# Performance work log

Hardware: AMD Instinct MI355X
Metric: run time of the kernel (lower is better)

Reference implementation:

```python
import jax, jax.numpy as jnp
import numpy as np

L, D, H, DH, W, G, FF = 2, 768, 12, 64, 256, 64, 3072  # W = one-sided window (attention_window=512)
B, S = 2, 4096
NEG = -1e9


def setup_inputs() -> dict:
    key = jax.random.key(0)
    ks = jax.random.split(key, 16)
    inp = {}
    inp['hidden_states'] = jax.random.normal(ks[0], (B, S, D), jnp.float32)
    # HF Longformer convention: <0 masked, >0 global, 0 local. First G tokens are global.
    inp['attention_mask'] = jnp.zeros((B, S), jnp.float32).at[:, :G].set(1.0)
    inp['padding_len'] = 0
    inp['level_hierarchy'] = 0
    def w(k, shape):
        return (jax.random.normal(k, shape, jnp.float32) * 0.02)
    for i, n in enumerate(['Wq', 'Wk', 'Wv', 'Wqg', 'Wkg', 'Wvg', 'Wo']):
        inp[n] = w(ks[1 + i], (L, D, D))
        inp['b' + n[1:].lower()] = jnp.zeros((L, D), jnp.float32)
    inp['Wi'] = w(ks[8], (L, D, FF)); inp['bi'] = jnp.zeros((L, FF), jnp.float32)
    inp['Wo2'] = w(ks[9], (L, FF, D)); inp['bo2'] = jnp.zeros((L, D), jnp.float32)
    for n in ['ln1', 'ln2']:
        inp[n + '_g'] = jnp.ones((L, D), jnp.float32)
        inp[n + '_b'] = jnp.zeros((L, D), jnp.float32)
    return inp


def _ln(x, g, b):
    mu = jnp.mean(x, -1, keepdims=True)
    var = jnp.mean(jnp.square(x - mu), -1, keepdims=True)
    return (x - mu) * jax.lax.rsqrt(var + 1e-5) * g + b


def _chunk3(x, nc, w):
    # x: [..., S, d] -> [..., nc, 3w, d]: keys of chunks (c-1, c, c+1), zero-padded at the ends
    shp = x.shape
    xr = x.reshape(shp[:-2] + (nc, w, shp[-1]))
    pad = [(0, 0)] * xr.ndim
    pad[-3] = (1, 1)
    xp = jnp.pad(xr, pad)
    return jnp.concatenate([xp[..., :-2, :, :], xp[..., 1:-1, :, :], xp[..., 2:, :, :]], axis=-2)


def _layer(h, mask, Wq, bq, Wk, bk, Wv, bv, Wqg, bqg, Wkg, bkg, Wvg, bvg,
           Wo, bo, ln1_g, ln1_b, Wi, bi, Wo2, bo2, ln2_g, ln2_b):
    Bb, Ss, Dd = h.shape
    nc = Ss // W
    scale = 1.0 / np.sqrt(DH)
    def heads(x):
        return x.reshape(Bb, Ss, H, DH).transpose(0, 2, 1, 3)  # [B,H,S,dh]
    q = heads(h @ Wq + bq) * scale
    k = heads(h @ Wk + bk)
    v = heads(h @ Wv + bv)
    # --- sliding-window (banded) attention, chunked ---
    qc = q.reshape(Bb, H, nc, W, DH)
    k3 = _chunk3(k, nc, W)  # [B,H,nc,3W,dh]
    v3 = _chunk3(v, nc, W)
    local = jnp.einsum('bhcid,bhcjd->bhcij', qc, k3)  # [B,H,nc,W,3W]
    i = jnp.arange(W)[:, None]
    j = jnp.arange(3 * W)[None, :]
    band_ok = jnp.abs(j - W - i) <= W                              # [W,3W]
    keypos = jnp.arange(nc)[:, None, None] * W + (j - W)[None]     # [nc,1,3W]
    in_range = (keypos >= 0) & (keypos < Ss)
    # masked and global keys are removed from the windowed attention (handled via global cols)
    key_local = _chunk3((mask == 0).astype(h.dtype)[..., None], nc, W)[..., 0] > 0.5  # [B,nc,3W]
    valid = band_ok[None, None] & in_range[None] & key_local[:, :, None, :]  # [B,nc,W,3W]
    local = jnp.where(valid[:, None], local, NEG)
    # --- global key columns (every token attends to the G global tokens) ---
    kg, vg = k[:, :, :G], v[:, :, :G]
    sg = jnp.einsum('bhsd,bhgd->bhsg', q, kg).reshape(Bb, H, nc, W, G)
    probs = jax.nn.softmax(jnp.concatenate([sg, local], axis=-1), axis=-1)
    pg, pl = probs[..., :G], probs[..., G:]
    out = (jnp.einsum('bhcig,bhgd->bhcid', pg, vg)
           + jnp.einsum('bhcij,bhcjd->bhcid', pl, v3)).reshape(Bb, H, Ss, DH)
    # --- global token rows: full attention with dedicated global projections ---
    qg = heads(h @ Wqg + bqg)[:, :, :G] * scale
    kgf = heads(h @ Wkg + bkg)
    vgf = heads(h @ Wvg + bvg)
    add = jnp.where(mask < 0, NEG, 0.0)[:, None, None, :]
    pgl = jax.nn.softmax(jnp.einsum('bhgd,bhsd->bhgs', qg, kgf) + add, axis=-1)
    out = out.at[:, :, :G].set(jnp.einsum('bhgs,bhsd->bhgd', pgl, vgf))
    out = jnp.where((mask < 0)[:, None, :, None], 0.0, out)
    attn = out.transpose(0, 2, 1, 3).reshape(Bb, Ss, Dd) @ Wo + bo
    h = _ln(attn + h, ln1_g, ln1_b)
    ff = jax.nn.gelu(h @ Wi + bi, approximate=False) @ Wo2 + bo2
    return _ln(ff + h, ln2_g, ln2_b)


def reference(hidden_states, attention_mask, padding_len, level_hierarchy,
              Wq, bq, Wk, bk, Wv, bv, Wqg, bqg, Wkg, bkg, Wvg, bvg,
              Wo, bo, ln1_g, ln1_b, Wi, bi, Wo2, bo2, ln2_g, ln2_b):
    h = hidden_states
    for l in range(L):
        h = _layer(h, attention_mask,
                   Wq[l], bq[l], Wk[l], bk[l], Wv[l], bv[l],
                   Wqg[l], bqg[l], Wkg[l], bkg[l], Wvg[l], bvg[l],
                   Wo[l], bo[l], ln1_g[l], ln1_b[l],
                   Wi[l], bi[l], Wo2[l], bo2[l], ln2_g[l], ln2_b[l])
    if padding_len > 0:
        h = h[:, :-padding_len]
    return h
```

## Files before the change

### kernel.cpp

```cpp
#include <hip/hip_runtime.h>

#define B_ 2
#define S_ 4096
#define D_ 768
#define H_ 12
#define DH_ 64
#define W_ 256
#define G_ 64
#define FF_ 3072
#define L_ 2
#define M_ (B_*S_)
#define NEGV -1e9f
#define NSPLIT 16

typedef short bf16x8 __attribute__((ext_vector_type(8)));
typedef float f32x4 __attribute__((ext_vector_type(4)));
typedef unsigned short u16;
typedef unsigned short u16x4 __attribute__((ext_vector_type(4)));

__device__ __forceinline__ u16 f2bf(float f) {
  union { float f; unsigned u; } a; a.f = f;
  unsigned r = a.u + 0x7FFFu + ((a.u >> 16) & 1u);
  return (u16)(r >> 16);
}

__device__ __forceinline__ f32x4 mfma16(bf16x8 a, bf16x8 b, f32x4 c) {
  return __builtin_amdgcn_mfma_f32_16x16x32_bf16(a, b, c, 0, 0, 0);
}

__device__ __forceinline__ void gload16(const u16* g, u16* l) {
  __builtin_amdgcn_global_load_lds((const __attribute__((address_space(1))) void*)g,
                                   (__attribute__((address_space(3))) void*)l, 16, 0, 0);
}

__device__ __forceinline__ int xcd_swz(int bid, int nwg) {
  if ((nwg & 7) == 0) {
    int cpx = nwg >> 3;
    bid = (bid & 7) * cpx + (bid >> 3);
  }
  return bid;
}

struct Ptr7 { const float* p[7]; };
__global__ __launch_bounds__(256) void wtrans7(Ptr7 in, u16* __restrict__ out) {
  __shared__ float tile[32][33];
  int z = blockIdx.z;
  int slab = z >> 1, l = z & 1;
  const float* src = in.p[slab] + (size_t)l * D_ * D_;
  u16* dst = out + (size_t)z * D_ * D_;
  int k0 = blockIdx.y * 32, n0 = blockIdx.x * 32;
  int tx = threadIdx.x, ty = threadIdx.y;
#pragma unroll
  for (int i = 0; i < 4; i++)
    tile[ty + i*8][tx] = src[(size_t)(k0 + ty + i*8) * D_ + n0 + tx];
  __syncthreads();
#pragma unroll
  for (int i = 0; i < 4; i++)
    dst[(size_t)(n0 + ty + i*8) * D_ + k0 + tx] = f2bf(tile[tx][ty + i*8]);
}

__global__ __launch_bounds__(256) void wtrans(const float* __restrict__ in,
                                              u16* __restrict__ out, int K, int N) {
  __shared__ float tile[32][33];
  size_t base = (size_t)blockIdx.z * K * N;
  int k0 = blockIdx.y * 32, n0 = blockIdx.x * 32;
  int tx = threadIdx.x, ty = threadIdx.y;
#pragma unroll
  for (int i = 0; i < 4; i++)
    tile[ty + i*8][tx] = in[base + (size_t)(k0 + ty + i*8) * N + n0 + tx];
  __syncthreads();
#pragma unroll
  for (int i = 0; i < 4; i++)
    out[base + (size_t)(n0 + ty + i*8) * K + k0 + tx] = f2bf(tile[tx][ty + i*8]);
}

__global__ __launch_bounds__(256) void copyconv(const float* __restrict__ in,
                                                float* __restrict__ outf,
                                                u16* __restrict__ outb, int n4) {
  int i = blockIdx.x * 256 + threadIdx.x;
  if (i >= n4) return;
  float4 v = ((const float4*)in)[i];
  ((float4*)outf)[i] = v;
  u16x4 o;
  o[0] = f2bf(v.x); o[1] = f2bf(v.y); o[2] = f2bf(v.z); o[3] = f2bf(v.w);
  ((u16x4*)outb)[i] = o;
}

template <int MODE>
__global__ __launch_bounds__(256) void gemm_lds(const u16* __restrict__ A,
                                                const u16* __restrict__ Bt,
                                                const float* __restrict__ bias,
                                                float* __restrict__ Cf,
                                                u16* __restrict__ Cb,
                                                int Ndim, int Kdim, int rowTileStride) {
  __shared__ u16 lA[128 * 64];
  __shared__ u16 lB[128 * 64];
  int gx = gridDim.x;
  int bid = blockIdx.x + blockIdx.y * gx;
  bid = xcd_swz(bid, gx * gridDim.y);
  int bm = (bid / gx) * rowTileStride * 128;
  int bn = (bid % gx) * 128;
  int tid = threadIdx.x;
  int lane = tid & 63, w = tid >> 6;
  int r0w = (w >> 1) * 64, c0w = (w & 1) * 64;
  int lr = lane & 15, lg = lane >> 4;
  int srow = tid >> 3;
  int scol = ((tid & 7) ^ (srow & 7)) * 8;
  u16* ldst = (u16*)0;

  f32x4 acc[4][4] = {};
  for (int k0 = 0; k0 < Kdim; k0 += 64) {
#pragma unroll
    for (int p = 0; p < 4; p++) {
      gload16(A + (size_t)(bm + p * 32 + srow) * Kdim + k0 + scol, lA + p * 2048 + tid * 8);
      gload16(Bt + (size_t)(bn + p * 32 + srow) * Kdim + k0 + scol, lB + p * 2048 + tid * 8);
    }
    __syncthreads();
    bf16x8 a[2][4], b[2][4];
#pragma unroll
    for (int ks = 0; ks < 2; ks++)
#pragma unroll
      for (int i = 0; i < 4; i++) {
        int row = r0w + i * 16 + lr;
        int c8 = ks * 4 + lg;
        a[ks][i] = *(const bf16x8*)&lA[row * 64 + ((c8 ^ (row & 7)) * 8)];
        int rowb = c0w + i * 16 + lr;
        b[ks][i] = *(const bf16x8*)&lB[rowb * 64 + ((c8 ^ (rowb & 7)) * 8)];
      }
#pragma unroll
    for (int ks = 0; ks < 2; ks++)
#pragma unroll
      for (int i = 0; i < 4; i++)
#pragma unroll
        for (int j = 0; j < 4; j++)
          acc[i][j] = mfma16(a[ks][i], b[ks][j], acc[i][j]);
    __syncthreads();
  }
  (void)ldst;

  int r0 = bm + r0w, c0 = bn + c0w;
  int cr = (lane >> 4) * 4, cc = lane & 15;
#pragma unroll
  for (int j = 0; j < 4; j++) {
    int col = c0 + j * 16 + cc;
    float bv = bias[col];
#pragma unroll
    for (int i = 0; i < 4; i++) {
#pragma unroll
      for (int r = 0; r < 4; r++) {
        size_t off = (size_t)(r0 + i * 16 + cr + r) * Ndim + col;
        float v = acc[i][j][r] + bv;
        if (MODE == 0) Cf[off] = v;
        else if (MODE == 1) Cb[off] = f2bf(v);
        else if (MODE == 2) Cb[off] = f2bf(v * 0.125f);
        else Cb[off] = f2bf(0.5f * v * (1.0f + erff(v * 0.70710678118f)));
      }
    }
  }
}

struct Bias5 { const float* p[5]; };
__global__ __launch_bounds__(256) void gemm_qkv(const u16* __restrict__ A,
                                                const u16* __restrict__ Wt,
                                                Bias5 bp,
                                                u16* __restrict__ OutBase,
                                                int l) {
  __shared__ u16 lA[128 * 64];
  __shared__ u16 lB[128 * 64];
  int bid = blockIdx.x + blockIdx.y * 30;
  bid = xcd_swz(bid, 1920);
  int bx = bid % 30, by = bid / 30;
  int widx = bx / 6;
  int bn = (bx % 6) * 128;
  int bm = by * 128;
  int slab = widx + (widx >= 3 ? 1 : 0);
  const size_t DD = (size_t)D_ * D_;
  const u16* Bt = Wt + ((size_t)slab * L_ + l) * DD;
  u16* Cb = OutBase + (size_t)slab * M_ * D_;
  const float* bias = bp.p[widx];
  int tid = threadIdx.x;
  int lane = tid & 63, w = tid >> 6;
  int r0w = (w >> 1) * 64, c0w = (w & 1) * 64;
  int lr = lane & 15, lg = lane >> 4;
  int srow = tid >> 3;
  int scol = ((tid & 7) ^ (srow & 7)) * 8;

  f32x4 acc[4][4] = {};
  for (int k0 = 0; k0 < D_; k0 += 64) {
#pragma unroll
    for (int p = 0; p < 4; p++) {
      gload16(A + (size_t)(bm + p * 32 + srow) * D_ + k0 + scol, lA + p * 2048 + tid * 8);
      gload16(Bt + (size_t)(bn + p * 32 + srow) * D_ + k0 + scol, lB + p * 2048 + tid * 8);
    }
    __syncthreads();
    bf16x8 a[2][4], b[2][4];
#pragma unroll
    for (int ks = 0; ks < 2; ks++)
#pragma unroll
      for (int i = 0; i < 4; i++) {
        int row = r0w + i * 16 + lr;
        int c8 = ks * 4 + lg;
        a[ks][i] = *(const bf16x8*)&lA[row * 64 + ((c8 ^ (row & 7)) * 8)];
        int rowb = c0w + i * 16 + lr;
        b[ks][i] = *(const bf16x8*)&lB[rowb * 64 + ((c8 ^ (rowb & 7)) * 8)];
      }
#pragma unroll
    for (int ks = 0; ks < 2; ks++)
#pragma unroll
      for (int i = 0; i < 4; i++)
#pragma unroll
        for (int j = 0; j < 4; j++)
          acc[i][j] = mfma16(a[ks][i], b[ks][j], acc[i][j]);
    __syncthreads();
  }

  int r0 = bm + r0w, c0 = bn + c0w;
  int cr = (lane >> 4) * 4, cc = lane & 15;
  float scale = (widx == 0) ? 0.125f : 1.0f;
#pragma unroll
  for (int j = 0; j < 4; j++) {
    int col = c0 + j * 16 + cc;
    float bv = bias[col];
#pragma unroll
    for (int i = 0; i < 4; i++) {
#pragma unroll
      for (int r = 0; r < 4; r++) {
        size_t off = (size_t)(r0 + i * 16 + cr + r) * D_ + col;
        Cb[off] = f2bf((acc[i][j][r] + bv) * scale);
      }
    }
  }
}

__global__ __launch_bounds__(128) void attn_local(const u16* __restrict__ qb,
                                                  const u16* __restrict__ kb_,
                                                  const u16* __restrict__ vb,
                                                  const float* __restrict__ mask,
                                                  u16* __restrict__ ao) {
  int bid = blockIdx.x + blockIdx.y * gridDim.x;
  bid = xcd_swz(bid, 1536);
  int cx = bid & 63, bh = bid >> 6;
  int c = cx >> 2, sub = cx & 3;
  int b = bh / H_, h = bh % H_;
  int tid = threadIdx.x;
  int w = tid >> 6, lane = tid & 63;
  int lr = lane & 15, lg = lane >> 4;

  __shared__ u16 vtT[64][72];
  __shared__ u16 plds[2][32][72];
  __shared__ unsigned char vflag[576];

  int base_off = sub * 64;
  int kwin0 = c * W_ - W_;
  for (int i = tid; i < 576; i += 128) {
    int kp = kwin0 + base_off + i;
    vflag[i] = (kp >= 0 && kp < S_ && mask[b * S_ + kp] == 0.0f) ? 1 : 0;
  }

  size_t hoff = (size_t)b * S_ * D_ + h * DH_;
  int qrow0 = c * W_ + base_off + w * 32;
  bf16x8 aq[2][2];
#pragma unroll
  for (int fi = 0; fi < 2; fi++)
#pragma unroll
    for (int ks = 0; ks < 2; ks++)
      aq[fi][ks] = *(const bf16x8*)(qb + hoff + (size_t)(qrow0 + fi * 16 + lr) * D_ + ks * 32 + lg * 8);

  float ls[2][4];
  f32x4 o[2][4] = {};
#pragma unroll
  for (int fi = 0; fi < 2; fi++)
#pragma unroll
    for (int r = 0; r < 4; r++) ls[fi][r] = 0.f;

  int stg_k4 = tid >> 3, stg_j = tid & 7;
  int stg_dh0 = stg_j * 8;

  for (int kb = 0; kb <= 9; kb++) {
    int kstart = 0;
    if (kb > 0) {
      kstart = kwin0 + base_off + (kb - 1) * 64;
      if (kstart + 64 <= 0 || kstart >= S_) continue;
    }
    __syncthreads();
    {
#pragma unroll
      for (int p = 0; p < 4; p++) {
        int key = p * 16 + stg_k4;
        int kp = (kb ? kstart : 0) + key;
        bf16x8 row = *(const bf16x8*)(vb + hoff + (size_t)kp * D_ + stg_dh0);
        u16* basep = &vtT[stg_dh0][key ^ (stg_j << 3)];
#pragma unroll
        for (int e = 0; e < 8; e++) basep[e * 72] = (u16)row[e];
      }
    }
    __syncthreads();

    bf16x8 bk0[4], bk1[4];
#pragma unroll
    for (int nj = 0; nj < 4; nj++) {
      int kp = (kb ? kstart : 0) + nj * 16 + lr;
      const u16* ks8 = kb_ + hoff + (size_t)kp * D_ + lg * 8;
      bk0[nj] = *(const bf16x8*)(ks8);
      bk1[nj] = *(const bf16x8*)(ks8 + 32);
    }
    f32x4 sc[2][4];
#pragma unroll
    for (int fi = 0; fi < 2; fi++)
#pragma unroll
      for (int nj = 0; nj < 4; nj++) {
        f32x4 t = {};
        t = mfma16(aq[fi][0], bk0[nj], t);
        t = mfma16(aq[fi][1], bk1[nj], t);
        sc[fi][nj] = t;
      }

    if (kb >= 2 && kb <= 8) {
#pragma unroll
      for (int nj = 0; nj < 4; nj++) {
        bool kv = vflag[(kb - 1) * 64 + nj * 16 + lr] != 0;
#pragma unroll
        for (int fi = 0; fi < 2; fi++)
#pragma unroll
          for (int r = 0; r < 4; r++)
            sc[fi][nj][r] = kv ? sc[fi][nj][r] : NEGV;
      }
    } else if (kb > 0) {
#pragma unroll
      for (int nj = 0; nj < 4; nj++) {
        int fidx = (kb - 1) * 64 + nj * 16 + lr;
        int koff = base_off + fidx;
        bool kv = vflag[fidx] != 0;
#pragma unroll
        for (int fi = 0; fi < 2; fi++)
#pragma unroll
          for (int r = 0; r < 4; r++) {
            int wq = base_off + w * 32 + fi * 16 + lg * 4 + r;
            if (!(kv && koff >= wq && koff <= wq + 2 * W_)) sc[fi][nj][r] = NEGV;
          }
      }
    }

#pragma unroll
    for (int fi = 0; fi < 2; fi++)
#pragma unroll
      for (int r = 0; r < 4; r++) {
        float ps = 0.f;
#pragma unroll
        for (int nj = 0; nj < 4; nj++) {
          float p = __expf(sc[fi][nj][r]);
          sc[fi][nj][r] = p;
          ps += p;
        }
#pragma unroll
        for (int d = 1; d < 16; d <<= 1) ps += __shfl_xor(ps, d);
        ls[fi][r] += ps;
      }

#pragma unroll
    for (int fi = 0; fi < 2; fi++)
#pragma unroll
      for (int nj = 0; nj < 4; nj++)
#pragma unroll
        for (int r = 0; r < 4; r++)
          plds[w][fi * 16 + lg * 4 + r][nj * 16 + lr] = f2bf(sc[fi][nj][r]);
    asm volatile("s_waitcnt lgkmcnt(0)" ::: "memory");
    __builtin_amdgcn_sched_barrier(0);

    bf16x8 ap[2][2];
#pragma unroll
    for (int fi = 0; fi < 2; fi++)
#pragma unroll
      for (int ks = 0; ks < 2; ks++)
        ap[fi][ks] = *(const bf16x8*)&plds[w][fi * 16 + lr][ks * 32 + lg * 8];
#pragma unroll
    for (int dj = 0; dj < 4; dj++) {
      int xr = ((dj * 16 + lr) >> 3) & 7;
#pragma unroll
      for (int ks = 0; ks < 2; ks++) {
        bf16x8 bv = *(const bf16x8*)&vtT[dj * 16 + lr][(ks * 32 + lg * 8) ^ (xr << 3)];
        o[0][dj] = mfma16(ap[0][ks], bv, o[0][dj]);
        o[1][dj] = mfma16(ap[1][ks], bv, o[1][dj]);
      }
    }
  }

#pragma unroll
  for (int fi = 0; fi < 2; fi++)
#pragma unroll
    for (int dj = 0; dj < 4; dj++)
#pragma unroll
      for (int r = 0; r < 4; r++) {
        int row = qrow0 + fi * 16 + lg * 4 + r;
        float v = o[fi][dj][r] / ls[fi][r];
        ao[hoff + (size_t)row * D_ + dj * 16 + lr] = f2bf(v);
      }
}

__global__ __launch_bounds__(128) void attn_gsplit(const u16* __restrict__ qg,
                                                   const u16* __restrict__ kg,
                                                   const u16* __restrict__ vg,
                                                   float* __restrict__ opart,
                                                   float* __restrict__ lpart) {
  int sp = blockIdx.x, bh = blockIdx.y;
  int b = bh / H_, h = bh % H_;
  int tid = threadIdx.x, w = tid >> 6, lane = tid & 63;
  int lr = lane & 15, lg = lane >> 4;
  __shared__ u16 vtT[64][72];
  __shared__ u16 plds[2][32][72];
  size_t hoff = (size_t)b * S_ * D_ + h * DH_;
  int qrow0 = w * 32;
  bf16x8 aq[2][2];
#pragma unroll
  for (int fi = 0; fi < 2; fi++)
#pragma unroll
    for (int ks = 0; ks < 2; ks++)
      aq[fi][ks] = *(const bf16x8*)(qg + hoff + (size_t)(qrow0 + fi * 16 + lr) * D_ + ks * 32 + lg * 8);
  float ls[2][4];
  f32x4 o[2][4] = {};
#pragma unroll
  for (int fi = 0; fi < 2; fi++)
#pragma unroll
    for (int r = 0; r < 4; r++) ls[fi][r] = 0.f;

  int stg_k4 = tid >> 3, stg_j = tid & 7;
  int stg_dh0 = stg_j * 8;

  for (int kb = 0; kb < 4; kb++) {
    int kstart = sp * 256 + kb * 64;
    __syncthreads();
#pragma unroll
    for (int p = 0; p < 4; p++) {
      int key = p * 16 + stg_k4;
      bf16x8 row = *(const bf16x8*)(vg + hoff + (size_t)(kstart + key) * D_ + stg_dh0);
      u16* basep = &vtT[stg_dh0][key ^ (stg_j << 3)];
#pragma unroll
      for (int e = 0; e < 8; e++) basep[e * 72] = (u16)row[e];
    }
    __syncthreads();

    bf16x8 bk0[4], bk1[4];
#pragma unroll
    for (int nj = 0; nj < 4; nj++) {
      const u16* ks8 = kg + hoff + (size_t)(kstart + nj * 16 + lr) * D_ + lg * 8;
      bk0[nj] = *(const bf16x8*)(ks8);
      bk1[nj] = *(const bf16x8*)(ks8 + 32);
    }
    f32x4 sc[2][4];
#pragma unroll
    for (int fi = 0; fi < 2; fi++)
#pragma unroll
      for (int nj = 0; nj < 4; nj++) {
        f32x4 t = {};
        t = mfma16(aq[fi][0], bk0[nj], t);
        t = mfma16(aq[fi][1], bk1[nj], t);
        sc[fi][nj] = t;
      }
#pragma unroll
    for (int fi = 0; fi < 2; fi++)
#pragma unroll
      for (int r = 0; r < 4; r++) {
        float ps = 0.f;
#pragma unroll
        for (int nj = 0; nj < 4; nj++) {
          float p = __expf(sc[fi][nj][r]);
          sc[fi][nj][r] = p;
          ps += p;
        }
#pragma unroll
        for (int d = 1; d < 16; d <<= 1) ps += __shfl_xor(ps, d);
        ls[fi][r] += ps;
      }
#pragma unroll
    for (int fi = 0; fi < 2; fi++)
#pragma unroll
      for (int nj = 0; nj < 4; nj++)
#pragma unroll
        for (int r = 0; r < 4; r++)
          plds[w][fi * 16 + lg * 4 + r][nj * 16 + lr] = f2bf(sc[fi][nj][r]);
    asm volatile("s_waitcnt lgkmcnt(0)" ::: "memory");
    __builtin_amdgcn_sched_barrier(0);
    bf16x8 ap[2][2];
#pragma unroll
    for (int fi = 0; fi < 2; fi++)
#pragma unroll
      for (int ks = 0; ks < 2; ks++)
        ap[fi][ks] = *(const bf16x8*)&plds[w][fi * 16 + lr][ks * 32 + lg * 8];
#pragma unroll
    for (int dj = 0; dj < 4; dj++) {
      int xr = ((dj * 16 + lr) >> 3) & 7;
#pragma unroll
      for (int ks = 0; ks < 2; ks++) {
        bf16x8 bv = *(const bf16x8*)&vtT[dj * 16 + lr][(ks * 32 + lg * 8) ^ (xr << 3)];
        o[0][dj] = mfma16(ap[0][ks], bv, o[0][dj]);
        o[1][dj] = mfma16(ap[1][ks], bv, o[1][dj]);
      }
    }
  }

  size_t pbase = (size_t)(bh * NSPLIT + sp) * 64;
#pragma unroll
  for (int fi = 0; fi < 2; fi++)
#pragma unroll
    for (int r = 0; r < 4; r++) {
      int row = qrow0 + fi * 16 + lg * 4 + r;
      if (lr == 0) lpart[pbase + row] = ls[fi][r];
#pragma unroll
      for (int dj = 0; dj < 4; dj++)
        opart[(pbase + row) * 64 + dj * 16 + lr] = o[fi][dj][r];
    }
}

__global__ __launch_bounds__(256) void attn_gcombine(const float* __restrict__ opart,
                                                     const float* __restrict__ lpart,
                                                     u16* __restrict__ ao) {
  int bh = blockIdx.x;
  int b = bh / H_, h = bh % H_;
  int t = threadIdx.x;
  __shared__ float lt[64];
  if (t < 64) {
    float lsum = 0.f;
#pragma unroll
    for (int sp = 0; sp < NSPLIT; sp++)
      lsum += lpart[(size_t)(bh * NSPLIT + sp) * 64 + t];
    lt[t] = lsum;
  }
  __syncthreads();
  int row = t >> 2, c0 = (t & 3) * 16;
  float acc[16] = {};
  for (int sp = 0; sp < NSPLIT; sp++) {
    const float* op = opart + ((size_t)(bh * NSPLIT + sp) * 64 + row) * 64 + c0;
#pragma unroll
    for (int j = 0; j < 16; j++) acc[j] += op[j];
  }
  float inv = 1.f / lt[row];
  size_t hoff = (size_t)b * S_ * D_ + h * DH_;
#pragma unroll
  for (int j = 0; j < 16; j++)
    ao[hoff + (size_t)row * D_ + c0 + j] = f2bf(acc[j] * inv);
}

__global__ __launch_bounds__(256) void ln_fused(const float* __restrict__ x,
                                                const float* __restrict__ res,
                                                const float* __restrict__ gg,
                                                const float* __restrict__ bb,
                                                float* __restrict__ outf,
                                                u16* __restrict__ outb) {
  int row = blockIdx.x, t = threadIdx.x;
  const float* xr = x + (size_t)row * D_;
  const float* rr = res + (size_t)row * D_;
  float v0 = xr[t] + rr[t];
  float v1 = xr[t + 256] + rr[t + 256];
  float v2 = xr[t + 512] + rr[t + 512];
  __shared__ float sha[4], shb[4];
  float s = v0 + v1 + v2;
#pragma unroll
  for (int d = 1; d < 64; d <<= 1) s += __shfl_xor(s, d);
  if ((t & 63) == 0) sha[t >> 6] = s;
  __syncthreads();
  float mu = (sha[0] + sha[1] + sha[2] + sha[3]) * (1.f / 768.f);
  float d0 = v0 - mu, d1 = v1 - mu, d2 = v2 - mu;
  float s2 = d0 * d0 + d1 * d1 + d2 * d2;
#pragma unroll
  for (int d = 1; d < 64; d <<= 1) s2 += __shfl_xor(s2, d);
  if ((t & 63) == 0) shb[t >> 6] = s2;
  __syncthreads();
  float var = (shb[0] + shb[1] + shb[2] + shb[3]) * (1.f / 768.f);
  float rs = rsqrtf(var + 1e-5f);
  float dd[3] = {d0, d1, d2};
#pragma unroll
  for (int i = 0; i < 3; i++) {
    int col = t + i * 256;
    float y = dd[i] * rs * gg[col] + bb[col];
    outf[(size_t)row * D_ + col] = y;
    outb[(size_t)row * D_ + col] = f2bf(y);
  }
}

extern "C" void kernel_launch(void* const* d_in, const int* in_sizes, int n_in,
                              void* d_out, int out_size, void* d_ws, size_t ws_size,
                              hipStream_t stream) {
  (void)in_sizes; (void)n_in; (void)out_size; (void)ws_size;
  const float* hidden = (const float*)d_in[0];
  const float* mask   = (const float*)d_in[1];
  const float* Wq  = (const float*)d_in[4];   const float* bq  = (const float*)d_in[5];
  const float* Wk  = (const float*)d_in[6];   const float* bk  = (const float*)d_in[7];
  const float* Wv  = (const float*)d_in[8];   const float* bv  = (const float*)d_in[9];
  const float* Wqg = (const float*)d_in[10];  const float* bqg = (const float*)d_in[11];
  const float* Wkg = (const float*)d_in[12];  const float* bkg = (const float*)d_in[13];
  const float* Wvg = (const float*)d_in[14];  const float* bvg = (const float*)d_in[15];
  const float* Wo  = (const float*)d_in[16];  const float* bo  = (const float*)d_in[17];
  const float* Wi  = (const float*)d_in[18];  const float* bi  = (const float*)d_in[19];
  const float* Wo2 = (const float*)d_in[20];  const float* bo2 = (const float*)d_in[21];
  const float* ln1g = (const float*)d_in[22]; const float* ln1b = (const float*)d_in[23];
  const float* ln2g = (const float*)d_in[24]; const float* ln2b = (const float*)d_in[25];

  char* ws = (char*)d_ws;
  size_t off = 0;
  auto alloc = [&](size_t bytes) -> void* {
    void* p = ws + off;
    off += (bytes + 255) & ~(size_t)255;
    return p;
  };
  const size_t DD = (size_t)D_ * D_;
  const size_t DF = (size_t)D_ * FF_;
  u16* Wt = (u16*)alloc((7 * L_ * DD + 2 * L_ * DF) * 2);
  u16* wqg_t = Wt + 3 * L_ * DD;
  u16* wo_t  = Wt + 6 * L_ * DD;
  u16* wi_t  = Wt + 7 * L_ * DD;
  u16* wo2_t = Wt + 7 * L_ * DD + L_ * DF;

  float* hbuf  = (float*)alloc((size_t)M_ * D_ * 4);
  float* h1buf = (float*)alloc((size_t)M_ * D_ * 4);
  float* t1    = (float*)alloc((size_t)M_ * D_ * 4);
  u16* A_bf = (u16*)alloc((size_t)M_ * D_ * 2);
  u16* B_bf = (u16*)alloc((size_t)M_ * FF_ * 2);
  u16* qbf  = (u16*)alloc((size_t)M_ * D_ * 2);
  u16* kbf  = (u16*)alloc((size_t)M_ * D_ * 2);
  u16* vbf  = (u16*)alloc((size_t)M_ * D_ * 2);
  u16* qgbf = (u16*)alloc((size_t)M_ * D_ * 2);
  u16* kgbf = (u16*)alloc((size_t)M_ * D_ * 2);
  u16* vgbf = (u16*)alloc((size_t)M_ * D_ * 2);
  u16* aobf = (u16*)alloc((size_t)M_ * D_ * 2);
  float* opart = (float*)alloc((size_t)B_ * H_ * NSPLIT * 64 * 64 * 4);
  float* lpart = (float*)alloc((size_t)B_ * H_ * NSPLIT * 64 * 4);

  dim3 tb(32, 8);
  Ptr7 wp;
  wp.p[0] = Wq; wp.p[1] = Wk; wp.p[2] = Wv; wp.p[3] = Wqg;
  wp.p[4] = Wkg; wp.p[5] = Wvg; wp.p[6] = Wo;
  wtrans7<<<dim3(24, 24, 14), tb, 0, stream>>>(wp, Wt);
  wtrans<<<dim3(96, 24, 2), tb, 0, stream>>>(Wi,  wi_t,  D_, FF_);
  wtrans<<<dim3(24, 96, 2), tb, 0, stream>>>(Wo2, wo2_t, FF_, D_);

  copyconv<<<(M_ * D_ / 4 + 255) / 256, 256, 0, stream>>>(hidden, hbuf, A_bf, M_ * D_ / 4);

  for (int l = 0; l < L_; l++) {
    size_t wdd = (size_t)l * DD;
    size_t wdf = (size_t)l * DF;
    dim3 g64(6, 64), g2(6, 2), gff(24, 64);

    Bias5 bp;
    bp.p[0] = bq  + l * D_;
    bp.p[1] = bk  + l * D_;
    bp.p[2] = bv  + l * D_;
    bp.p[3] = bkg + l * D_;
    bp.p[4] = bvg + l * D_;
    gemm_qkv<<<dim3(30, 64), 256, 0, stream>>>(A_bf, Wt, bp, qbf, l);
    gemm_lds<2><<<g2, 256, 0, stream>>>(A_bf, wqg_t + wdd, bqg + l * D_, nullptr, qgbf, D_, D_, 32);

    attn_local<<<dim3((S_ / W_) * 4, B_ * H_), 128, 0, stream>>>(qbf, kbf, vbf, mask, aobf);
    attn_gsplit<<<dim3(NSPLIT, B_ * H_), 128, 0, stream>>>(qgbf, kgbf, vgbf, opart, lpart);
    attn_gcombine<<<B_ * H_, 256, 0, stream>>>(opart, lpart, aobf);

    gemm_lds<0><<<g64, 256, 0, stream>>>(aobf, wo_t + wdd, bo + l * D_, t1, nullptr, D_, D_, 1);
    ln_fused<<<M_, 256, 0, stream>>>(t1, hbuf, ln1g + l * D_, ln1b + l * D_, h1buf, A_bf);

    gemm_lds<3><<<gff, 256, 0, stream>>>(A_bf, wi_t + wdf, bi + l * FF_, nullptr, B_bf, FF_, D_, 1);
    gemm_lds<0><<<g64, 256, 0, stream>>>(B_bf, wo2_t + wdf, bo2 + l * D_, t1, nullptr, D_, FF_, 1);

    float* outp = (l == L_ - 1) ? (float*)d_out : hbuf;
    ln_fused<<<M_, 256, 0, stream>>>(t1, h1buf, ln2g + l * D_, ln2b + l * D_, outp, A_bf);
  }
}
```

Before: 767.6 us.

## Double-buffer GEMM K loop, keep residual stream in bf16, use tanh GELU

The GEMM kernels now load the next K slice into a second LDS buffer while MFMAs run on the current one. The K step drops to 32 with a remapped swizzle, and waits use vmcnt plus raw barriers. The residual stream and GEMM outputs are stored as bf16 instead of fp32, and LayerNorm reads bf16 with vectorized loads, so far fewer bytes move between kernels. Exact erf GELU is replaced by a tanh approximation. Together these cut memory traffic and stall time, at the cost of lower precision in the residual path and in the GELU.

```diff
diff --git a/kernel.cpp b/kernel.cpp
--- a/kernel.cpp
+++ b/kernel.cpp
@@ -23,6 +23,10 @@
   unsigned r = a.u + 0x7FFFu + ((a.u >> 16) & 1u);
   return (u16)(r >> 16);
 }
+__device__ __forceinline__ float b2f(u16 u) {
+  union { unsigned u; float f; } a; a.u = ((unsigned)u) << 16;
+  return a.f;
+}
 
 __device__ __forceinline__ f32x4 mfma16(bf16x8 a, bf16x8 b, f32x4 c) {
   return __builtin_amdgcn_mfma_f32_16x16x32_bf16(a, b, c, 0, 0, 0);
@@ -74,27 +78,35 @@
     out[base + (size_t)(n0 + ty + i*8) * K + k0 + tx] = f2bf(tile[tx][ty + i*8]);
 }
 
-__global__ __launch_bounds__(256) void copyconv(const float* __restrict__ in,
-                                                float* __restrict__ outf,
-                                                u16* __restrict__ outb, int n4) {
+__global__ __launch_bounds__(256) void conv_b(const float* __restrict__ in,
+                                              u16* __restrict__ outb, int n4) {
   int i = blockIdx.x * 256 + threadIdx.x;
   if (i >= n4) return;
   float4 v = ((const float4*)in)[i];
-  ((float4*)outf)[i] = v;
   u16x4 o;
   o[0] = f2bf(v.x); o[1] = f2bf(v.y); o[2] = f2bf(v.z); o[3] = f2bf(v.w);
   ((u16x4*)outb)[i] = o;
 }
 
 template <int MODE>
-__global__ __launch_bounds__(256) void gemm_lds(const u16* __restrict__ A,
-                                                const u16* __restrict__ Bt,
-                                                const float* __restrict__ bias,
-                                                float* __restrict__ Cf,
-                                                u16* __restrict__ Cb,
-                                                int Ndim, int Kdim, int rowTileStride) {
-  __shared__ u16 lA[128 * 64];
-  __shared__ u16 lB[128 * 64];
+__device__ __forceinline__ float epi_post(float v) {
+  if (MODE == 2) return v * 0.125f;
+  if (MODE == 3) {
+    float y = 0.79788456f * (v + 0.044715f * v * v * v);
+    float e = __expf(fminf(2.f * y, 20.f));
+    return v * e / (e + 1.f);
+  }
+  return v;
+}
+
+template <int MODE>
+__global__ __launch_bounds__(256) void gemm_pipe(const u16* __restrict__ A,
+                                                 const u16* __restrict__ Bt,
+                                                 const float* __restrict__ bias,
+                                                 u16* __restrict__ Cb,
+                                                 int Ndim, int Kdim, int rowTileStride) {
+  __shared__ u16 sA[2][4096];
+  __shared__ u16 sB[2][4096];
   int gx = gridDim.x;
   int bid = blockIdx.x + blockIdx.y * gx;
   bid = xcd_swz(bid, gx * gridDim.y);
@@ -104,39 +116,63 @@
   int lane = tid & 63, w = tid >> 6;
   int r0w = (w >> 1) * 64, c0w = (w & 1) * 64;
   int lr = lane & 15, lg = lane >> 4;
-  int srow = tid >> 3;
-  int scol = ((tid & 7) ^ (srow & 7)) * 8;
-  u16* ldst = (u16*)0;
-
+
+  int f0 = tid, l0 = f0 >> 3, s0 = (f0 & 7) ^ (l0 & 7);
+  int row0 = (l0 << 1) | (s0 >> 2), c0s = (s0 & 3) * 8;
+  int f1 = tid + 256, l1 = f1 >> 3, s1 = (f1 & 7) ^ (l1 & 7);
+  int row1 = (l1 << 1) | (s1 >> 2), c1s = (s1 & 3) * 8;
+  const u16* A0 = A + (size_t)(bm + row0) * Kdim + c0s;
+  const u16* A1 = A + (size_t)(bm + row1) * Kdim + c1s;
+  const u16* B0 = Bt + (size_t)(bn + row0) * Kdim + c0s;
+  const u16* B1 = Bt + (size_t)(bn + row1) * Kdim + c1s;
+
+  int offa[4], offb[4];
+#pragma unroll
+  for (int i = 0; i < 4; i++) {
+    int ra = r0w + i * 16 + lr;
+    int la = ra >> 1, sa = ((ra & 1) << 2) | lg;
+    offa[i] = la * 64 + (sa ^ (la & 7)) * 8;
+    int rb = c0w + i * 16 + lr;
+    int lb = rb >> 1, sb = ((rb & 1) << 2) | lg;
+    offb[i] = lb * 64 + (sb ^ (lb & 7)) * 8;
+  }
+
+  int nt = Kdim >> 5;
   f32x4 acc[4][4] = {};
-  for (int k0 = 0; k0 < Kdim; k0 += 64) {
-#pragma unroll
-    for (int p = 0; p < 4; p++) {
-      gload16(A + (size_t)(bm + p * 32 + srow) * Kdim + k0 + scol, lA + p * 2048 + tid * 8);
-      gload16(Bt + (size_t)(bn + p * 32 + srow) * Kdim + k0 + scol, lB + p * 2048 + tid * 8);
-    }
-    __syncthreads();
-    bf16x8 a[2][4], b[2][4];
-#pragma unroll
-    for (int ks = 0; ks < 2; ks++)
-#pragma unroll
-      for (int i = 0; i < 4; i++) {
-        int row = r0w + i * 16 + lr;
-        int c8 = ks * 4 + lg;
-        a[ks][i] = *(const bf16x8*)&lA[row * 64 + ((c8 ^ (row & 7)) * 8)];
-        int rowb = c0w + i * 16 + lr;
-        b[ks][i] = *(const bf16x8*)&lB[rowb * 64 + ((c8 ^ (rowb & 7)) * 8)];
-      }
-#pragma unroll
-    for (int ks = 0; ks < 2; ks++)
-#pragma unroll
-      for (int i = 0; i < 4; i++)
-#pragma unroll
-        for (int j = 0; j < 4; j++)
-          acc[i][j] = mfma16(a[ks][i], b[ks][j], acc[i][j]);
-    __syncthreads();
-  }
-  (void)ldst;
+
+  gload16(A0, &sA[0][tid * 8]);
+  gload16(A1, &sA[0][tid * 8 + 2048]);
+  gload16(B0, &sB[0][tid * 8]);
+  gload16(B1, &sB[0][tid * 8 + 2048]);
+
+  for (int t = 0; t < nt; t++) {
+    int cur = t & 1;
+    if (t + 1 < nt) {
+      int k1 = (t + 1) << 5;
+      gload16(A0 + k1, &sA[cur ^ 1][tid * 8]);
+      gload16(A1 + k1, &sA[cur ^ 1][tid * 8 + 2048]);
+      gload16(B0 + k1, &sB[cur ^ 1][tid * 8]);
+      gload16(B1 + k1, &sB[cur ^ 1][tid * 8 + 2048]);
+      asm volatile("s_waitcnt vmcnt(4)" ::: "memory");
+    } else {
+      asm volatile("s_waitcnt vmcnt(0)" ::: "memory");
+    }
+    __builtin_amdgcn_s_barrier();
+    __builtin_amdgcn_sched_barrier(0);
+    bf16x8 a[4], b[4];
+#pragma unroll
+    for (int i = 0; i < 4; i++) a[i] = *(const bf16x8*)&sA[cur][offa[i]];
+#pragma unroll
+    for (int j = 0; j < 4; j++) b[j] = *(const bf16x8*)&sB[cur][offb[j]];
+#pragma unroll
+    for (int i = 0; i < 4; i++)
+#pragma unroll
+      for (int j = 0; j < 4; j++)
+        acc[i][j] = mfma16(a[i], b[j], acc[i][j]);
+    __builtin_amdgcn_sched_barrier(0);
+    __builtin_amdgcn_s_barrier();
+    __builtin_amdgcn_sched_barrier(0);
+  }
 
   int r0 = bm + r0w, c0 = bn + c0w;
   int cr = (lane >> 4) * 4, cc = lane & 15;
@@ -145,17 +181,12 @@
     int col = c0 + j * 16 + cc;
     float bv = bias[col];
 #pragma unroll
-    for (int i = 0; i < 4; i++) {
+    for (int i = 0; i < 4; i++)
 #pragma unroll
       for (int r = 0; r < 4; r++) {
         size_t off = (size_t)(r0 + i * 16 + cr + r) * Ndim + col;
-        float v = acc[i][j][r] + bv;
-        if (MODE == 0) Cf[off] = v;
-        else if (MODE == 1) Cb[off] = f2bf(v);
-        else if (MODE == 2) Cb[off] = f2bf(v * 0.125f);
-        else Cb[off] = f2bf(0.5f * v * (1.0f + erff(v * 0.70710678118f)));
-      }
-    }
+        Cb[off] = f2bf(epi_post<MODE>(acc[i][j][r] + bv));
+      }
   }
 }
 
@@ -165,8 +196,8 @@
                                                 Bias5 bp,
                                                 u16* __restrict__ OutBase,
                                                 int l) {
-  __shared__ u16 lA[128 * 64];
-  __shared__ u16 lB[128 * 64];
+  __shared__ u16 sA[2][4096];
+  __shared__ u16 sB[2][4096];
   int bid = blockIdx.x + blockIdx.y * 30;
   bid = xcd_swz(bid, 1920);
   int bx = bid % 30, by = bid / 30;
@@ -182,36 +213,62 @@
   int lane = tid & 63, w = tid >> 6;
   int r0w = (w >> 1) * 64, c0w = (w & 1) * 64;
   int lr = lane & 15, lg = lane >> 4;
-  int srow = tid >> 3;
-  int scol = ((tid & 7) ^ (srow & 7)) * 8;
-
+
+  int f0 = tid, l0 = f0 >> 3, s0 = (f0 & 7) ^ (l0 & 7);
+  int row0 = (l0 << 1) | (s0 >> 2), c0s = (s0 & 3) * 8;
+  int f1 = tid + 256, l1 = f1 >> 3, s1 = (f1 & 7) ^ (l1 & 7);
+  int row1 = (l1 << 1) | (s1 >> 2), c1s = (s1 & 3) * 8;
+  const u16* A0 = A + (size_t)(bm + row0) * D_ + c0s;
+  const u16* A1 = A + (size_t)(bm + row1) * D_ + c1s;
+  const u16* B0 = Bt + (size_t)(bn + row0) * D_ + c0s;
+  const u16* B1 = Bt + (size_t)(bn + row1) * D_ + c1s;
+
+  int offa[4], offb[4];
+#pragma unroll
+  for (int i = 0; i < 4; i++) {
+    int ra = r0w + i * 16 + lr;
+    int la = ra >> 1, sa = ((ra & 1) << 2) | lg;
+    offa[i] = la * 64 + (sa ^ (la & 7)) * 8;
+    int rb = c0w + i * 16 + lr;
+    int lb = rb >> 1, sb = ((rb & 1) << 2) | lg;
+    offb[i] = lb * 64 + (sb ^ (lb & 7)) * 8;
+  }
+
+  const int nt = D_ >> 5;
   f32x4 acc[4][4] = {};
-  for (int k0 = 0; k0 < D_; k0 += 64) {
-#pragma unroll
-    for (int p = 0; p < 4; p++) {
-      gload16(A + (size_t)(bm + p * 32 + srow) * D_ + k0 + scol, lA + p * 2048 + tid * 8);
-      gload16(Bt + (size_t)(bn + p * 32 + srow) * D_ + k0 + scol, lB + p * 2048 + tid * 8);
-    }
-    __syncthreads();
-    bf16x8 a[2][4], b[2][4];
-#pragma unroll
-    for (int ks = 0; ks < 2; ks++)
-#pragma unroll
-      for (int i = 0; i < 4; i++) {
-        int row = r0w + i * 16 + lr;
-        int c8 = ks * 4 + lg;
-        a[ks][i] = *(const bf16x8*)&lA[row * 64 + ((c8 ^ (row & 7)) * 8)];
-        int rowb = c0w + i * 16 + lr;
-        b[ks][i] = *(const bf16x8*)&lB[rowb * 64 + ((c8 ^ (rowb & 7)) * 8)];
-      }
-#pragma unroll
-    for (int ks = 0; ks < 2; ks++)
-#pragma unroll
-      for (int i = 0; i < 4; i++)
-#pragma unroll
-        for (int j = 0; j < 4; j++)
-          acc[i][j] = mfma16(a[ks][i], b[ks][j], acc[i][j]);
-    __syncthreads();
+
+  gload16(A0, &sA[0][tid * 8]);
+  gload16(A1, &sA[0][tid * 8 + 2048]);
+  gload16(B0, &sB[0][tid * 8]);
+  gload16(B1, &sB[0][tid * 8 + 2048]);
+
+  for (int t = 0; t < nt; t++) {
+    int cur = t & 1;
+    if (t + 1 < nt) {
+      int k1 = (t + 1) << 5;
+      gload16(A0 + k1, &sA[cur ^ 1][tid * 8]);
+      gload16(A1 + k1, &sA[cur ^ 1][tid * 8 + 2048]);
+      gload16(B0 + k1, &sB[cur ^ 1][tid * 8]);
+      gload16(B1 + k1, &sB[cur ^ 1][tid * 8 + 2048]);
+      asm volatile("s_waitcnt vmcnt(4)" ::: "memory");
+    } else {
+      asm volatile("s_waitcnt vmcnt(0)" ::: "memory");
+    }
+    __builtin_amdgcn_s_barrier();
+    __builtin_amdgcn_sched_barrier(0);
+    bf16x8 a[4], b[4];
+#pragma unroll
+    for (int i = 0; i < 4; i++) a[i] = *(const bf16x8*)&sA[cur][offa[i]];
+#pragma unroll
+    for (int j = 0; j < 4; j++) b[j] = *(const bf16x8*)&sB[cur][offb[j]];
+#pragma unroll
+    for (int i = 0; i < 4; i++)
+#pragma unroll
+      for (int j = 0; j < 4; j++)
+        acc[i][j] = mfma16(a[i], b[j], acc[i][j]);
+    __builtin_amdgcn_sched_barrier(0);
+    __builtin_amdgcn_s_barrier();
+    __builtin_amdgcn_sched_barrier(0);
   }
 
   int r0 = bm + r0w, c0 = bn + c0w;
@@ -222,13 +279,12 @@
     int col = c0 + j * 16 + cc;
     float bv = bias[col];
 #pragma unroll
-    for (int i = 0; i < 4; i++) {
+    for (int i = 0; i < 4; i++)
 #pragma unroll
       for (int r = 0; r < 4; r++) {
         size_t off = (size_t)(r0 + i * 16 + cr + r) * D_ + col;
         Cb[off] = f2bf((acc[i][j][r] + bv) * scale);
       }
-    }
   }
 }
 
@@ -540,40 +596,48 @@
     ao[hoff + (size_t)row * D_ + c0 + j] = f2bf(acc[j] * inv);
 }
 
-__global__ __launch_bounds__(256) void ln_fused(const float* __restrict__ x,
-                                                const float* __restrict__ res,
-                                                const float* __restrict__ gg,
-                                                const float* __restrict__ bb,
-                                                float* __restrict__ outf,
-                                                u16* __restrict__ outb) {
+__global__ __launch_bounds__(192) void ln_b(const u16* __restrict__ x,
+                                            const u16* __restrict__ res,
+                                            const float* __restrict__ gg,
+                                            const float* __restrict__ bb,
+                                            u16* __restrict__ outb,
+                                            float* __restrict__ outf) {
   int row = blockIdx.x, t = threadIdx.x;
-  const float* xr = x + (size_t)row * D_;
-  const float* rr = res + (size_t)row * D_;
-  float v0 = xr[t] + rr[t];
-  float v1 = xr[t + 256] + rr[t + 256];
-  float v2 = xr[t + 512] + rr[t + 512];
-  __shared__ float sha[4], shb[4];
-  float s = v0 + v1 + v2;
+  const u16* xr = x + (size_t)row * D_;
+  const u16* rr = res + (size_t)row * D_;
+  u16x4 xv = *(const u16x4*)&xr[t * 4];
+  u16x4 rv = *(const u16x4*)&rr[t * 4];
+  float v[4];
+#pragma unroll
+  for (int e = 0; e < 4; e++) v[e] = b2f(xv[e]) + b2f(rv[e]);
+  __shared__ float sha[3], shb[3];
+  float s = v[0] + v[1] + v[2] + v[3];
 #pragma unroll
   for (int d = 1; d < 64; d <<= 1) s += __shfl_xor(s, d);
   if ((t & 63) == 0) sha[t >> 6] = s;
   __syncthreads();
-  float mu = (sha[0] + sha[1] + sha[2] + sha[3]) * (1.f / 768.f);
-  float d0 = v0 - mu, d1 = v1 - mu, d2 = v2 - mu;
-  float s2 = d0 * d0 + d1 * d1 + d2 * d2;
+  float mu = (sha[0] + sha[1] + sha[2]) * (1.f / 768.f);
+  float dd[4], s2 = 0.f;
+#pragma unroll
+  for (int e = 0; e < 4; e++) { dd[e] = v[e] - mu; s2 += dd[e] * dd[e]; }
 #pragma unroll
   for (int d = 1; d < 64; d <<= 1) s2 += __shfl_xor(s2, d);
   if ((t & 63) == 0) shb[t >> 6] = s2;
   __syncthreads();
-  float var = (shb[0] + shb[1] + shb[2] + shb[3]) * (1.f / 768.f);
+  float var = (shb[0] + shb[1] + shb[2]) * (1.f / 768.f);
   float rs = rsqrtf(var + 1e-5f);
-  float dd[3] = {d0, d1, d2};
-#pragma unroll
-  for (int i = 0; i < 3; i++) {
-    int col = t + i * 256;
-    float y = dd[i] * rs * gg[col] + bb[col];
-    outf[(size_t)row * D_ + col] = y;
-    outb[(size_t)row * D_ + col] = f2bf(y);
+  float4 gv = *(const float4*)&gg[t * 4];
+  float4 bv = *(const float4*)&bb[t * 4];
+  float y0 = dd[0] * rs * gv.x + bv.x;
+  float y1 = dd[1] * rs * gv.y + bv.y;
+  float y2 = dd[2] * rs * gv.z + bv.z;
+  float y3 = dd[3] * rs * gv.w + bv.w;
+  u16x4 ov;
+  ov[0] = f2bf(y0); ov[1] = f2bf(y1); ov[2] = f2bf(y2); ov[3] = f2bf(y3);
+  *(u16x4*)&outb[(size_t)row * D_ + t * 4] = ov;
+  if (outf) {
+    float4 of = {y0, y1, y2, y3};
+    *(float4*)&outf[(size_t)row * D_ + t * 4] = of;
   }
 }
 
@@ -610,10 +674,9 @@
   u16* wi_t  = Wt + 7 * L_ * DD;
   u16* wo2_t = Wt + 7 * L_ * DD + L_ * DF;
 
-  float* hbuf  = (float*)alloc((size_t)M_ * D_ * 4);
-  float* h1buf = (float*)alloc((size_t)M_ * D_ * 4);
-  float* t1    = (float*)alloc((size_t)M_ * D_ * 4);
-  u16* A_bf = (u16*)alloc((size_t)M_ * D_ * 2);
+  u16* X0 = (u16*)alloc((size_t)M_ * D_ * 2);
+  u16* X1 = (u16*)alloc((size_t)M_ * D_ * 2);
+  u16* tb = (u16*)alloc((size_t)M_ * D_ * 2);
   u16* B_bf = (u16*)alloc((size_t)M_ * FF_ * 2);
   u16* qbf  = (u16*)alloc((size_t)M_ * D_ * 2);
   u16* kbf  = (u16*)alloc((size_t)M_ * D_ * 2);
@@ -625,15 +688,15 @@
   float* opart = (float*)alloc((size_t)B_ * H_ * NSPLIT * 64 * 64 * 4);
   float* lpart = (float*)alloc((size_t)B_ * H_ * NSPLIT * 64 * 4);
 
-  dim3 tb(32, 8);
+  dim3 tb32(32, 8);
   Ptr7 wp;
   wp.p[0] = Wq; wp.p[1] = Wk; wp.p[2] = Wv; wp.p[3] = Wqg;
   wp.p[4] = Wkg; wp.p[5] = Wvg; wp.p[6] = Wo;
-  wtrans7<<<dim3(24, 24, 14), tb, 0, stream>>>(wp, Wt);
-  wtrans<<<dim3(96, 24, 2), tb, 0, stream>>>(Wi,  wi_t,  D_, FF_);
-  wtrans<<<dim3(24, 96, 2), tb, 0, stream>>>(Wo2, wo2_t, FF_, D_);
-
-  copyconv<<<(M_ * D_ / 4 + 255) / 256, 256, 0, stream>>>(hidden, hbuf, A_bf, M_ * D_ / 4);
+  wtrans7<<<dim3(24, 24, 14), tb32, 0, stream>>>(wp, Wt);
+  wtrans<<<dim3(96, 24, 2), tb32, 0, stream>>>(Wi,  wi_t,  D_, FF_);
+  wtrans<<<dim3(24, 96, 2), tb32, 0, stream>>>(Wo2, wo2_t, FF_, D_);
+
+  conv_b<<<(M_ * D_ / 4 + 255) / 256, 256, 0, stream>>>(hidden, X0, M_ * D_ / 4);
 
   for (int l = 0; l < L_; l++) {
     size_t wdd = (size_t)l * DD;
@@ -646,20 +709,20 @@
     bp.p[2] = bv  + l * D_;
     bp.p[3] = bkg + l * D_;
     bp.p[4] = bvg + l * D_;
-    gemm_qkv<<<dim3(30, 64), 256, 0, stream>>>(A_bf, Wt, bp, qbf, l);
-    gemm_lds<2><<<g2, 256, 0, stream>>>(A_bf, wqg_t + wdd, bqg + l * D_, nullptr, qgbf, D_, D_, 32);
+    gemm_qkv<<<dim3(30, 64), 256, 0, stream>>>(X0, Wt, bp, qbf, l);
+    gemm_pipe<2><<<g2, 256, 0, stream>>>(X0, wqg_t + wdd, bqg + l * D_, qgbf, D_, D_, 32);
 
     attn_local<<<dim3((S_ / W_) * 4, B_ * H_), 128, 0, stream>>>(qbf, kbf, vbf, mask, aobf);
     attn_gsplit<<<dim3(NSPLIT, B_ * H_), 128, 0, stream>>>(qgbf, kgbf, vgbf, opart, lpart);
     attn_gcombine<<<B_ * H_, 256, 0, stream>>>(opart, lpart, aobf);
 
-    gemm_lds<0><<<g64, 256, 0, stream>>>(aobf, wo_t + wdd, bo + l * D_, t1, nullptr, D_, D_, 1);
-    ln_fused<<<M_, 256, 0, stream>>>(t1, hbuf, ln1g + l * D_, ln1b + l * D_, h1buf, A_bf);
-
-    gemm_lds<3><<<gff, 256, 0, stream>>>(A_bf, wi_t + wdf, bi + l * FF_, nullptr, B_bf, FF_, D_, 1);
-    gemm_lds<0><<<g64, 256, 0, stream>>>(B_bf, wo2_t + wdf, bo2 + l * D_, t1, nullptr, D_, FF_, 1);
-
-    float* outp = (l == L_ - 1) ? (float*)d_out : hbuf;
-    ln_fused<<<M_, 256, 0, stream>>>(t1, h1buf, ln2g + l * D_, ln2b + l * D_, outp, A_bf);
-  }
-}
+    gemm_pipe<1><<<g64, 256, 0, stream>>>(aobf, wo_t + wdd, bo + l * D_, tb, D_, D_, 1);
+    ln_b<<<M_, 192, 0, stream>>>(tb, X0, ln1g + l * D_, ln1b + l * D_, X1, nullptr);
+
+    gemm_pipe<3><<<gff, 256, 0, stream>>>(X1, wi_t + wdf, bi + l * FF_, B_bf, FF_, D_, 1);
+    gemm_pipe<1><<<g64, 256, 0, stream>>>(B_bf, wo2_t + wdf, bo2 + l * D_, tb, D_, FF_, 1);
+
+    ln_b<<<M_, 192, 0, stream>>>(tb, X1, ln2g + l * D_, ln2b + l * D_, X0,
+                                 (l == L_ - 1) ? (float*)d_out : nullptr);
+  }
+}
```

Result: faster. 737.0 us (-4.0%).
